# Performance work log

Measured on AMD Instinct MI355X. Metric: run time of the kernel, lower is better.

The kernel has to match this reference:

```python
import jax, jax.numpy as jnp
import numpy as np

# Mamba2 hyperparameters
D_MODEL = 768
D_STATE = 64
D_CONV = 4
EXPAND = 2
HEADDIM = 64
CHUNK = 64
D_INNER = EXPAND * D_MODEL            # 1536
NHEADS = D_INNER // HEADDIM           # 24
D_IN_PROJ = 2 * D_INNER + 2 * D_STATE + NHEADS  # 3224
CONV_DIM = D_INNER + 2 * D_STATE      # 1664
B_SZ = 8
SEQ = 4096  # multiple of CHUNK -> no padding branch


def setup_inputs() -> dict:
    key = jax.random.key(0)
    ks = jax.random.split(key, 6)
    u = jax.random.normal(ks[0], (B_SZ, SEQ, D_MODEL), jnp.float32)
    # fan-in scaled weights (matches nn.Linear/Conv1d default init scale)
    W_in = jax.random.normal(ks[1], (D_IN_PROJ, D_MODEL), jnp.float32) / np.sqrt(D_MODEL).astype(np.float32)
    conv_w = jax.random.normal(ks[2], (CONV_DIM, 1, D_CONV), jnp.float32) / np.sqrt(D_CONV).astype(np.float32)
    conv_b = jnp.zeros((CONV_DIM,), jnp.float32)
    dt_bias = jax.random.uniform(ks[3], (NHEADS,), jnp.float32, -4.0, 1.0)  # nn.init.uniform_(-4, 1)
    A_log = jnp.full((NHEADS,), -np.log(2.0), jnp.float32)                  # nn.init.constant_(-log 2)
    D_param = jnp.ones((NHEADS,), jnp.float32)
    norm_w = jnp.ones((D_INNER,), jnp.float32)
    W_out = jax.random.normal(ks[4], (D_MODEL, D_INNER), jnp.float32) / np.sqrt(D_INNER).astype(np.float32)
    return dict(u=u, W_in=W_in, conv_w=conv_w, conv_b=conv_b, dt_bias=dt_bias,
                A_log=A_log, D_param=D_param, norm_w=norm_w, W_out=W_out)


def _segsum(x):
    """Stable segment sum: out[..., i, j] = sum_{j < k <= i} x[..., k]; -inf above diagonal."""
    T = x.shape[-1]
    lower_strict = jnp.tril(jnp.ones((T, T), bool), -1)
    xe = jnp.where(lower_strict, x[..., :, None], 0.0)   # broadcast x over last (col) axis
    s = jnp.cumsum(xe, axis=-2)
    lower = jnp.tril(jnp.ones((T, T), bool), 0)
    return jnp.where(lower, s, -jnp.inf)


def _ssd(x, A, B, C, chunk):
    """Chunked SSD. x:(b,L,h,p)  A:(b,L,h)  B,C:(b,L,1,n)."""
    b, L, h, p = x.shape
    c = L // chunk
    n = B.shape[-1]
    x = x.reshape(b, c, chunk, h, p)
    A = A.reshape(b, c, chunk, h).transpose(0, 3, 1, 2)   # b h c l
    B = B.reshape(b, c, chunk, 1, n)
    C = C.reshape(b, c, chunk, 1, n)
    A_cs = jnp.cumsum(A, axis=-1)                          # b h c l
    # intra-chunk (diagonal) term
    Lmat = jnp.exp(_segsum(A))                             # b h c l s
    Y_diag = jnp.einsum('bclhn,bcshn,bhcls,bcshp->bclhp', C, B, Lmat, x)
    # per-chunk states
    decay_states = jnp.exp(A_cs[..., -1:] - A_cs)          # b h c l
    states = jnp.einsum('bclhn,bhcl,bclhp->bchpn', B, decay_states, x)
    states = jnp.concatenate([jnp.zeros_like(states[:, :1]), states], axis=1)  # b (c+1) h p n
    # inter-chunk recurrence
    A_last = jnp.pad(A_cs[..., -1], ((0, 0), (0, 0), (1, 0)))  # b h (c+1)
    decay_chunk = jnp.exp(_segsum(A_last))                     # b h (c+1) (c+1)
    new_states = jnp.einsum('bhzc,bchpn->bzhpn', decay_chunk, states)
    states = new_states[:, :-1]                                # b c h p n
    # off-diagonal (state-to-output) term
    Y_off = jnp.einsum('bclhn,bchpn,bhcl->bclhp', C, states, jnp.exp(A_cs))
    return (Y_diag + Y_off).reshape(b, L, h, p)


def reference(u, W_in, conv_w, conv_b, dt_bias, A_log, D_param, norm_w, W_out):
    b, L, _ = u.shape  # L % CHUNK == 0, so pad branch is a no-op
    zxbcdt = u @ W_in.T                                    # (b, L, D_IN_PROJ)
    z = zxbcdt[..., :D_INNER]
    xBC = zxbcdt[..., D_INNER:D_INNER + CONV_DIM]
    dt = jax.nn.softplus(zxbcdt[..., D_INNER + CONV_DIM:] + dt_bias)  # (b, L, h)
    # causal depthwise conv1d (torch pads both sides by d_conv-1 then slices [:L] == left pad)
    xBC = jax.lax.conv_general_dilated(
        xBC.transpose(0, 2, 1), conv_w, window_strides=(1,),
        padding=[(D_CONV - 1, 0)], dimension_numbers=('NCH', 'OIH', 'NCH'),
        feature_group_count=CONV_DIM)
    xBC = jax.nn.silu(xBC.transpose(0, 2, 1) + conv_b)     # (b, L, CONV_DIM)
    x = xBC[..., :D_INNER].reshape(b, L, NHEADS, HEADDIM)
    Bm = xBC[..., D_INNER:D_INNER + D_STATE][:, :, None, :]  # (b, L, 1, n)
    Cm = xBC[..., D_INNER + D_STATE:][:, :, None, :]
    A = -jnp.exp(A_log)                                    # (h,)
    Y = _ssd(x * dt[..., None], A * dt, Bm, Cm, CHUNK)
    y = Y + x * D_param[:, None]                           # skip term
    y = y.reshape(b, L, D_INNER)
    # gated RMSNorm: x * silu(z), then rmsnorm * weight
    y = y * jax.nn.silu(z)
    y = y * jax.lax.rsqrt(jnp.mean(y * y, axis=-1, keepdims=True) + 1e-5) * norm_w
    return y @ W_out.T
```

## Files before the change

### kernel.cpp

```cpp
#include <hip/hip_runtime.h>
#include <stdint.h>

typedef unsigned short u16;
typedef __bf16 bf16x8 __attribute__((ext_vector_type(8)));
typedef float f32x4 __attribute__((ext_vector_type(4)));
typedef unsigned short u16x8 __attribute__((ext_vector_type(8)));
typedef unsigned short u16x4 __attribute__((ext_vector_type(4)));
typedef __attribute__((address_space(1))) unsigned int gu32;
typedef __attribute__((address_space(3))) unsigned int lu32;

__device__ __forceinline__ float bf2f(u16 u){ unsigned int v=((unsigned int)u)<<16; float f; __builtin_memcpy(&f,&v,4); return f; }
__device__ __forceinline__ u16 f2bf(float f){ unsigned int v; __builtin_memcpy(&v,&f,4); v += 0x7fffu + ((v>>16)&1u); return (u16)(v>>16); }
__device__ __forceinline__ void glds16(const void* g, void* l){
  __builtin_amdgcn_global_load_lds((gu32*)g, (lu32*)l, 16, 0, 0);
}

__global__ __launch_bounds__(256) void k_cast(const float* __restrict__ in, u16* __restrict__ out, int n4){
  int i = blockIdx.x*256 + threadIdx.x;
  if (i >= n4) return;
  const f32x4 v = *(const f32x4*)(in + (size_t)i*4);
  u16x4 o; o.x=f2bf(v.x); o.y=f2bf(v.y); o.z=f2bf(v.z); o.w=f2bf(v.w);
  *(u16x4*)(out + (size_t)i*4) = o;
}

__global__ __launch_bounds__(256) void k_cast_pad(const float* __restrict__ in, u16* __restrict__ out){
  int i = blockIdx.x*256 + threadIdx.x;
  int e0 = i*4;
  int row = e0 / 768;
  int col = e0 - row*768;
  u16x4 o;
  if (row < 3224){
    const f32x4 v = *(const f32x4*)(in + (size_t)row*768 + col);
    o.x=f2bf(v.x); o.y=f2bf(v.y); o.z=f2bf(v.z); o.w=f2bf(v.w);
  } else { o.x=0; o.y=0; o.z=0; o.w=0; }
  *(u16x4*)(out + e0) = o;
}

template<int K, int NT, int NH, int EPI>
__global__ __launch_bounds__(256,4) void k_gemm(
    const u16* __restrict__ A, const u16* __restrict__ Bw,
    u16* __restrict__ o_z, u16* __restrict__ o_xbc, float* __restrict__ o_dt,
    const float* __restrict__ dt_bias, float* __restrict__ o_f32)
{
  __shared__ __align__(16) u16 Alds[8192];
  __shared__ __align__(16) u16 Blds[8192];
  const int tid = threadIdx.x;
  const int wave = tid>>6, lane = tid&63;
  constexpr int NPH = NT / NH;
  const int bid = (int)blockIdx.x;
  const int x = bid & 7;
  const int q = bid >> 3;
  const int pass = q / (32*NPH);
  const int rem  = q % (32*NPH);
  const int m0 = ((x<<5) + rem/NPH) << 7;
  const int n0 = (pass*NPH + rem%NPH) << 7;
  const int wr = (wave>>1)<<6, wc = (wave&1)<<6;
  const int srow = tid>>3, sc0 = (tid&7)<<3;
  const int lo16 = lane&15, hi = lane>>4;
  f32x4 acc[4][4] = {};
  for (int k0 = 0; k0 < K; k0 += 64){
    #pragma unroll
    for (int i = 0; i < 4; ++i){
      const int row = (i<<5) + srow;
      const int scol = sc0 ^ ((row&7)<<3);
      glds16(A  + (size_t)(m0+row)*K + k0 + scol, &Alds[(i<<11) + (wave<<9)]);
      glds16(Bw + (size_t)(n0+row)*K + k0 + scol, &Blds[(i<<11) + (wave<<9)]);
    }
    __syncthreads();
    #pragma unroll
    for (int kk = 0; kk < 2; ++kk){
      const int kb = (kk<<5) + (hi<<3);
      bf16x8 af[4], bfv[4];
      #pragma unroll
      for (int m = 0; m < 4; ++m){
        const int r = wr + (m<<4) + lo16;
        af[m] = *(const bf16x8*)&Alds[(r<<6) + (kb ^ ((r&7)<<3))];
      }
      #pragma unroll
      for (int n = 0; n < 4; ++n){
        const int r = wc + (n<<4) + lo16;
        bfv[n] = *(const bf16x8*)&Blds[(r<<6) + (kb ^ ((r&7)<<3))];
      }
      #pragma unroll
      for (int m = 0; m < 4; ++m)
      #pragma unroll
      for (int n = 0; n < 4; ++n)
        acc[m][n] = __builtin_amdgcn_mfma_f32_16x16x32_bf16(af[m], bfv[n], acc[m][n], 0,0,0);
    }
    __syncthreads();
  }
  #pragma unroll
  for (int m = 0; m < 4; ++m)
  #pragma unroll
  for (int n = 0; n < 4; ++n)
  #pragma unroll
  for (int i = 0; i < 4; ++i){
    const int gr = m0 + wr + (m<<4) + (hi<<2) + i;
    const int gc = n0 + wc + (n<<4) + lo16;
    const float v = acc[m][n][i];
    if constexpr (EPI == 0){
      if (gc < 1536)      o_z[(size_t)gr*1536 + gc] = f2bf(v);
      else if (gc < 3200) o_xbc[(size_t)gr*1664 + (gc-1536)] = f2bf(v);
      else if (gc < 3224){
        const float t = v + dt_bias[gc-3200];
        o_dt[(size_t)(gc-3200)*32768 + gr] = (t > 20.f) ? t : log1pf(__expf(t));
      }
    } else {
      o_f32[(size_t)gr*768 + gc] = v;
    }
  }
}

__global__ __launch_bounds__(256) void k_conv(
    const u16* __restrict__ xbc, const float* __restrict__ cw, const float* __restrict__ cb,
    const float* __restrict__ dtT,
    u16* __restrict__ xT, u16* __restrict__ Bn, u16* __restrict__ BT, u16* __restrict__ Cn)
{
  const int idx = blockIdx.x*256 + threadIdx.x;
  if (idx >= 4096*208) return;
  const int g  = idx % 208;
  const int pt = idx / 208;
  const int ch0 = g << 3;
  const int m0 = pt << 3;
  const int l0 = m0 & 4095;
  float wgt[8][4], bias8[8];
  #pragma unroll
  for (int j = 0; j < 8; ++j){
    const f32x4 wv = *(const f32x4*)(cw + (size_t)(ch0+j)*4);
    wgt[j][0]=wv.x; wgt[j][1]=wv.y; wgt[j][2]=wv.z; wgt[j][3]=wv.w;
    bias8[j] = cb[ch0+j];
  }
  float acc[8][8];
  #pragma unroll
  for (int p = 0; p < 8; ++p)
  #pragma unroll
  for (int j = 0; j < 8; ++j) acc[p][j] = bias8[j];
  #pragma unroll
  for (int r = -3; r < 8; ++r){
    const int ls = l0 + r;
    if (ls < 0) continue;
    const u16x8 v = *(const u16x8*)(xbc + (size_t)(m0+r)*1664 + ch0);
    float xf[8];
    #pragma unroll
    for (int j = 0; j < 8; ++j) xf[j] = bf2f(v[j]);
    #pragma unroll
    for (int t = 0; t < 4; ++t){
      const int p = r + 3 - t;
      if (p < 0 || p > 7) continue;
      #pragma unroll
      for (int j = 0; j < 8; ++j) acc[p][j] += xf[j] * wgt[j][t];
    }
  }
  #pragma unroll
  for (int p = 0; p < 8; ++p)
  #pragma unroll
  for (int j = 0; j < 8; ++j){ const float s = acc[p][j]; acc[p][j] = s / (1.f + __expf(-s)); }

  const int b = m0 >> 12;
  const int cch = l0 >> 6;
  const int lr0 = l0 & 63;
  if (ch0 < 1536){
    const int h = ch0 >> 6, p0 = ch0 & 63;
    const f32x4 d0 = *(const f32x4*)(dtT + (size_t)h*32768 + m0);
    const f32x4 d1 = *(const f32x4*)(dtT + (size_t)h*32768 + m0 + 4);
    const float dtl[8] = {d0.x,d0.y,d0.z,d0.w,d1.x,d1.y,d1.z,d1.w};
    const size_t rb = (size_t)(b*24+h)*64;
    #pragma unroll
    for (int j = 0; j < 8; ++j){
      const int row = p0 + j;
      u16x8 o;
      #pragma unroll
      for (int p = 0; p < 8; ++p) o[p] = f2bf(acc[p][j] * dtl[p]);
      *(u16x8*)(xT + (rb + row)*4096 + (size_t)cch*64 + (lr0 ^ ((row&7)<<3))) = o;
    }
  } else if (ch0 < 1600){
    const int n0 = ch0 - 1536;
    const size_t tb = ((size_t)(b*64 + cch))*4096;
    #pragma unroll
    for (int p = 0; p < 8; ++p){
      const int lr = lr0 + p;
      u16x8 o;
      #pragma unroll
      for (int j = 0; j < 8; ++j) o[j] = f2bf(acc[p][j]);
      *(u16x8*)(Bn + tb + lr*64 + (n0 ^ ((lr&7)<<3))) = o;
    }
    #pragma unroll
    for (int j = 0; j < 8; ++j){
      const int row = n0 + j;
      u16x8 o;
      #pragma unroll
      for (int p = 0; p < 8; ++p) o[p] = f2bf(acc[p][j]);
      *(u16x8*)(BT + tb + row*64 + (lr0 ^ ((row&7)<<3))) = o;
    }
  } else {
    const int n0 = ch0 - 1600;
    const size_t tb = ((size_t)(b*64 + cch))*4096;
    #pragma unroll
    for (int p = 0; p < 8; ++p){
      const int lr = lr0 + p;
      u16x8 o;
      #pragma unroll
      for (int j = 0; j < 8; ++j) o[j] = f2bf(acc[p][j]);
      *(u16x8*)(Cn + tb + lr*64 + (n0 ^ ((lr&7)<<3))) = o;
    }
  }
}

__global__ __launch_bounds__(512,1) void k_ssd(
    const u16* __restrict__ xT, const u16* __restrict__ Bn, const u16* __restrict__ BT,
    const u16* __restrict__ Cn, const float* __restrict__ dtT, const float* __restrict__ A_log,
    const float* __restrict__ Dp, u16* __restrict__ yo)
{
  __shared__ __align__(16) u16 tiles[2][4][4096];
  __shared__ __align__(16) u16 Ml[4096];
  __shared__ __align__(16) u16 Sbf[2][4096];
  const int tid = threadIdx.x, wave = tid>>6, lane = tid&63;
  const int sg = wave & 3, hf = wave >> 2;
  const int lo16 = lane&15, hi = lane>>4;
  const int w16 = sg<<4, hi4 = hi<<2;
  const int b = blockIdx.x / 24, h = blockIdx.x % 24;
  const float Ah = -__expf(A_log[h]);
  const float Dh = Dp[h];
  for (int i = tid; i < 8192; i += 512) ((u16*)Sbf)[i] = 0;
  f32x4 Sreg[2] = {};
  const size_t xTg  = (size_t)(b*24+h)*64*4096;
  const size_t bcg  = (size_t)b*64*4096;
  const size_t dtg0 = (size_t)h*32768 + (size_t)b*4096;
  const size_t yb   = (size_t)b*4096*1536 + (size_t)h*64;

  auto stage = [&](int buf, int c){
    u16* dst = &tiles[buf][sg][0];
    if (sg == 0){
      const u16* g0 = xT + xTg + (size_t)c*64 + (size_t)(lane>>3)*4096 + (lane&7)*8;
      #pragma unroll
      for (int s = 0; s < 4; ++s){
        const int sx = (hf<<2) + s;
        glds16(g0 + (size_t)sx*32768, dst + sx*512);
      }
    } else {
      const u16* src = (sg==1 ? Bn : sg==2 ? BT : Cn) + bcg + (size_t)c*4096 + lane*8;
      #pragma unroll
      for (int s = 0; s < 4; ++s){
        const int sx = (hf<<2) + s;
        glds16(src + sx*512, dst + sx*512);
      }
    }
  };

  float dtc = dtT[dtg0 + lane];
  stage(0, 0);

  for (int c = 0; c < 64; ++c){
    float s = Ah * dtc;
    #pragma unroll
    for (int o = 1; o < 64; o <<= 1){ const float t = __shfl_up(s, o); if (lane >= o) s += t; }
    const float Alast = __shfl(s, 63);
    const float lam  = __expf(Alast);
    const float decl = __expf(Alast - s);
    const float elv  = __expf(s);
    float dtn = 0.f;
    if (c < 63){
      dtn = dtT[dtg0 + (size_t)(c+1)*64 + lane];
      stage((c+1)&1, c+1);
    }
    if (c == 0)       asm volatile("s_waitcnt vmcnt(5) lgkmcnt(0)" ::: "memory");
    else if (c == 63) asm volatile("s_waitcnt vmcnt(2) lgkmcnt(0)" ::: "memory");
    else              asm volatile("s_waitcnt vmcnt(7) lgkmcnt(0)" ::: "memory");
    __builtin_amdgcn_s_barrier();

    const u16* tx = &tiles[c&1][0][0];
    const u16* tb = &tiles[c&1][1][0];
    const u16* tt = &tiles[c&1][2][0];
    const u16* tc = &tiles[c&1][3][0];
    const u16* Sr = &Sbf[c&1][0];
    u16*       Sw = &Sbf[(c+1)&1][0];

    f32x4 accG[2] = {};
    bf16x8 bfC[2][2];
    #pragma unroll
    for (int kk = 0; kk < 2; ++kk){
      const int kb = (kk<<5) + (hi<<3);
      const int rA = w16 + lo16;
      const bf16x8 aB = *(const bf16x8*)&tb[(rA<<6) + (kb ^ ((rA&7)<<3))];
      #pragma unroll
      for (int ti = 0; ti < 2; ++ti){
        const int t = (hf<<1) + ti;
        const int rb = (t<<4) + lo16;
        bfC[kk][ti] = *(const bf16x8*)&tc[(rb<<6) + (kb ^ ((rb&7)<<3))];
        accG[ti] = __builtin_amdgcn_mfma_f32_16x16x32_bf16(aB, bfC[kk][ti], accG[ti], 0,0,0);
      }
    }
    float As_i[4];
    #pragma unroll
    for (int i = 0; i < 4; ++i) As_i[i] = __shfl(s, w16 + hi4 + i);
    #pragma unroll
    for (int ti = 0; ti < 2; ++ti){
      const int t = (hf<<1) + ti;
      const int l = (t<<4) + lo16;
      const float Al  = __shfl(s, l);
      const float dtl = __shfl(dtc, l);
      u16x4 ov;
      #pragma unroll
      for (int i = 0; i < 4; ++i){
        const int si = w16 + hi4 + i;
        float v = 0.f;
        if (si <= l) v = accG[ti][i] * __expf(Al - As_i[i]);
        if (si == l) v += Dh / dtl;
        ov[i] = f2bf(v);
      }
      *(u16x4*)&Ml[(l<<6) + ((w16 + hi4) ^ ((l&7)<<3))] = ov;
    }
    asm volatile("s_waitcnt lgkmcnt(0)" ::: "memory");
    __builtin_amdgcn_s_barrier();

    f32x4 aYd[2] = {}, aYo[2] = {}, aS[2] = {};
    #pragma unroll
    for (int kk = 0; kk < 2; ++kk){
      const int kb = (kk<<5) + (hi<<3);
      const int rA = w16 + lo16;
      const int oA = (rA<<6) + (kb ^ ((rA&7)<<3));
      const bf16x8 aX = *(const bf16x8*)&tx[oA];
      const bf16x8 aSb= *(const bf16x8*)&Sr[oA];
      const u16x8 aBTu= *(const u16x8*)&tt[oA];
      u16x8 aBTs;
      #pragma unroll
      for (int j = 0; j < 8; ++j) aBTs[j] = f2bf(bf2f(aBTu[j]) * __shfl(decl, kb + j));
      const bf16x8 aBT = *(const bf16x8*)&aBTs;
      #pragma unroll
      for (int ti = 0; ti < 2; ++ti){
        const int t = (hf<<1) + ti;
        const int rb = (t<<4) + lo16;
        const int o = (rb<<6) + (kb ^ ((rb&7)<<3));
        const bf16x8 bM = *(const bf16x8*)&Ml[o];
        const bf16x8 bX = *(const bf16x8*)&tx[o];
        aYd[ti] = __builtin_amdgcn_mfma_f32_16x16x32_bf16(aX,  bM,         aYd[ti], 0,0,0);
        aYo[ti] = __builtin_amdgcn_mfma_f32_16x16x32_bf16(aSb, bfC[kk][ti], aYo[ti], 0,0,0);
        aS[ti]  = __builtin_amdgcn_mfma_f32_16x16x32_bf16(aBT, bX,         aS[ti],  0,0,0);
      }
    }
    #pragma unroll
    for (int ti = 0; ti < 2; ++ti){
      const int t = (hf<<1) + ti;
      const int p = (t<<4) + lo16;
      u16x4 sv;
      #pragma unroll
      for (int i = 0; i < 4; ++i){
        const float nv = Sreg[ti][i] * lam + aS[ti][i];
        Sreg[ti][i] = nv;
        sv[i] = f2bf(nv);
      }
      *(u16x4*)&Sw[(p<<6) + ((w16 + hi4) ^ ((p&7)<<3))] = sv;
    }
    #pragma unroll
    for (int ti = 0; ti < 2; ++ti){
      const int t = (hf<<1) + ti;
      const int l = (t<<4) + lo16;
      const float elt = __shfl(elv, l);
      u16x4 ov;
      #pragma unroll
      for (int i = 0; i < 4; ++i) ov[i] = f2bf(aYd[ti][i] + elt * aYo[ti][i]);
      *(u16x4*)(yo + yb + (size_t)((c<<6)+l)*1536 + w16 + hi4) = ov;
    }
    dtc = dtn;
  }
}

__global__ __launch_bounds__(192) void k_gnorm(
    const u16* __restrict__ y, const u16* __restrict__ z,
    const float* __restrict__ nw, u16* __restrict__ out)
{
  __shared__ float red[3];
  const int m = blockIdx.x, t = threadIdx.x;
  const size_t base = (size_t)m*1536 + t*8;
  const u16x8 yv = *(const u16x8*)(y + base);
  const u16x8 zv = *(const u16x8*)(z + base);
  float vals[8]; float ss = 0.f;
  #pragma unroll
  for (int j = 0; j < 8; ++j){
    const float zf = bf2f(zv[j]);
    const float v = bf2f(yv[j]) * zf / (1.f + __expf(-zf));
    vals[j] = v; ss += v*v;
  }
  #pragma unroll
  for (int off = 32; off > 0; off >>= 1) ss += __shfl_down(ss, off);
  if ((t & 63) == 0) red[t>>6] = ss;
  __syncthreads();
  const float sc = rsqrtf((red[0]+red[1]+red[2]) * (1.f/1536.f) + 1e-5f);
  u16x8 o;
  #pragma unroll
  for (int j = 0; j < 8; ++j) o[j] = f2bf(vals[j] * sc * nw[t*8+j]);
  *(u16x8*)(out + base) = o;
}

extern "C" void kernel_launch(void* const* d_in, const int* in_sizes, int n_in,
                              void* d_out, int out_size, void* d_ws, size_t ws_size,
                              hipStream_t stream)
{
  const float* u       = (const float*)d_in[0];
  const float* W_in    = (const float*)d_in[1];
  const float* conv_w  = (const float*)d_in[2];
  const float* conv_b  = (const float*)d_in[3];
  const float* dt_bias = (const float*)d_in[4];
  const float* A_log   = (const float*)d_in[5];
  const float* D_param = (const float*)d_in[6];
  const float* norm_w  = (const float*)d_in[7];
  const float* W_out   = (const float*)d_in[8];
  (void)in_sizes; (void)n_in; (void)out_size;
  if (ws_size < (size_t)379715584) return;

  char* w = (char*)d_ws;
  size_t off = 0;
  auto alloc = [&](size_t bytes)->void*{ void* p = w + off; off += (bytes + 255) & ~(size_t)255; return p; };
  u16* ubf    = (u16*)alloc(50331648);
  u16* winbf  = (u16*)alloc(5111808);
  u16* woutbf = (u16*)alloc(2359296);
  u16* zbf    = (u16*)alloc(100663296);
  u16* xbcbf  = (u16*)alloc(109051904);
  float* dtT  = (float*)alloc(3145728);
  u16* xTb    = (u16*)alloc(100663296);
  u16* Bnb    = (u16*)alloc(4194304);
  u16* Cnb    = (u16*)alloc(4194304);
  u16* BTb    = ubf;
  u16* yssd   = xbcbf;
  u16* ynorm  = xTb;

  k_cast<<<24576, 256, 0, stream>>>(u, ubf, 6291456);
  k_cast_pad<<<2496, 256, 0, stream>>>(W_in, winbf);
  k_cast<<<1152, 256, 0, stream>>>(W_out, woutbf, 294912);
  k_gemm<768,26,2,0><<<6656, 256, 0, stream>>>(ubf, winbf, zbf, xbcbf, dtT, dt_bias, nullptr);
  k_conv<<<3328, 256, 0, stream>>>(xbcbf, conv_w, conv_b, dtT, xTb, Bnb, BTb, Cnb);
  k_ssd<<<192, 512, 0, stream>>>(xTb, Bnb, BTb, Cnb, dtT, A_log, D_param, yssd);
  k_gnorm<<<32768, 192, 0, stream>>>(yssd, zbf, norm_w, ynorm);
  k_gemm<1536,6,1,1><<<1536, 256, 0, stream>>>(ynorm, woutbf, nullptr, nullptr, nullptr, nullptr, (float*)d_out);
}
```

Measured before the change: 638.2 us.

## Fuse gated RMSNorm into SSD epilogue and out-projection GEMM row scaling

Removes the separate gated-norm kernel. The SSD epilogue now loads z, applies the silu gate and writes per-head partial sums of squares. A small kernel reduces these to per-row rsqrt scales, which the output GEMM epilogue applies, while norm_w is folded into the bf16 W_out cast. This saves a full read and write pass over the 100MB activation, at the cost of extra z loads and LDS traffic inside the latency-bound SSD loop, plus adjusted waitcnt counts.

```diff
diff --git a/kernel.cpp b/kernel.cpp
--- a/kernel.cpp
+++ b/kernel.cpp
@@ -34,6 +34,26 @@
     o.x=f2bf(v.x); o.y=f2bf(v.y); o.z=f2bf(v.z); o.w=f2bf(v.w);
   } else { o.x=0; o.y=0; o.z=0; o.w=0; }
   *(u16x4*)(out + e0) = o;
+}
+
+__global__ __launch_bounds__(256) void k_cast_wout(const float* __restrict__ in, const float* __restrict__ nw, u16* __restrict__ out){
+  int i = blockIdx.x*256 + threadIdx.x;
+  if (i >= 294912) return;
+  const int e0 = i*4;
+  const int k = e0 % 1536;
+  const f32x4 v = *(const f32x4*)(in + e0);
+  const f32x4 w4 = *(const f32x4*)(nw + k);
+  u16x4 o; o.x=f2bf(v.x*w4.x); o.y=f2bf(v.y*w4.y); o.z=f2bf(v.z*w4.z); o.w=f2bf(v.w*w4.w);
+  *(u16x4*)(out + e0) = o;
+}
+
+__global__ __launch_bounds__(256) void k_scale(const float* __restrict__ ps, float* __restrict__ sc){
+  const int m = blockIdx.x*256 + threadIdx.x;
+  const float* p = ps + (size_t)m*24;
+  float s = 0.f;
+  #pragma unroll
+  for (int j = 0; j < 6; ++j){ const f32x4 v = *(const f32x4*)(p + j*4); s += v.x+v.y+v.z+v.w; }
+  sc[m] = rsqrtf(s*(1.f/1536.f) + 1e-5f);
 }
 
 template<int K, int NT, int NH, int EPI>
@@ -106,7 +126,7 @@
         o_dt[(size_t)(gc-3200)*32768 + gr] = (t > 20.f) ? t : log1pf(__expf(t));
       }
     } else {
-      o_f32[(size_t)gr*768 + gc] = v;
+      o_f32[(size_t)gr*768 + gc] = v * o_dt[gr];
     }
   }
 }
@@ -209,11 +229,13 @@
 __global__ __launch_bounds__(512,1) void k_ssd(
     const u16* __restrict__ xT, const u16* __restrict__ Bn, const u16* __restrict__ BT,
     const u16* __restrict__ Cn, const float* __restrict__ dtT, const float* __restrict__ A_log,
-    const float* __restrict__ Dp, u16* __restrict__ yo)
+    const float* __restrict__ Dp, const u16* __restrict__ zg, float* __restrict__ psum,
+    u16* __restrict__ yo)
 {
   __shared__ __align__(16) u16 tiles[2][4][4096];
   __shared__ __align__(16) u16 Ml[4096];
   __shared__ __align__(16) u16 Sbf[2][4096];
+  __shared__ float ps_lds[2][64][4];
   const int tid = threadIdx.x, wave = tid>>6, lane = tid&63;
   const int sg = wave & 3, hf = wave >> 2;
   const int lo16 = lane&15, hi = lane>>4;
@@ -227,6 +249,7 @@
   const size_t bcg  = (size_t)b*64*4096;
   const size_t dtg0 = (size_t)h*32768 + (size_t)b*4096;
   const size_t yb   = (size_t)b*4096*1536 + (size_t)h*64;
+  const size_t pbase = (size_t)b*4096*24 + h;
 
   auto stage = [&](int buf, int c){
     u16* dst = &tiles[buf][sg][0];
@@ -251,6 +274,12 @@
   stage(0, 0);
 
   for (int c = 0; c < 64; ++c){
+    u16x4 zv[2];
+    #pragma unroll
+    for (int ti = 0; ti < 2; ++ti){
+      const int l = (((hf<<1)+ti)<<4) + lo16;
+      zv[ti] = *(const u16x4*)(zg + yb + (size_t)((c<<6)+l)*1536 + w16 + hi4);
+    }
     float s = Ah * dtc;
     #pragma unroll
     for (int o = 1; o < 64; o <<= 1){ const float t = __shfl_up(s, o); if (lane >= o) s += t; }
@@ -263,10 +292,15 @@
       dtn = dtT[dtg0 + (size_t)(c+1)*64 + lane];
       stage((c+1)&1, c+1);
     }
-    if (c == 0)       asm volatile("s_waitcnt vmcnt(5) lgkmcnt(0)" ::: "memory");
-    else if (c == 63) asm volatile("s_waitcnt vmcnt(2) lgkmcnt(0)" ::: "memory");
-    else              asm volatile("s_waitcnt vmcnt(7) lgkmcnt(0)" ::: "memory");
+    if (c == 0)       asm volatile("s_waitcnt vmcnt(6) lgkmcnt(0)" ::: "memory");
+    else if (c == 63) asm volatile("s_waitcnt vmcnt(3) lgkmcnt(0)" ::: "memory");
+    else              asm volatile("s_waitcnt vmcnt(8) lgkmcnt(0)" ::: "memory");
     __builtin_amdgcn_s_barrier();
+
+    if (wave == 7 && c > 0){
+      const f32x4 pv = *(const f32x4*)&ps_lds[(c&1)^1][lane][0];
+      psum[pbase + (size_t)(((c-1)<<6) + lane)*24] = pv.x+pv.y+pv.z+pv.w;
+    }
 
     const u16* tx = &tiles[c&1][0][0];
     const u16* tb = &tiles[c&1][1][0];
@@ -357,39 +391,27 @@
       const int l = (t<<4) + lo16;
       const float elt = __shfl(elv, l);
       u16x4 ov;
-      #pragma unroll
-      for (int i = 0; i < 4; ++i) ov[i] = f2bf(aYd[ti][i] + elt * aYo[ti][i]);
+      float pss = 0.f;
+      #pragma unroll
+      for (int i = 0; i < 4; ++i){
+        const float zf = bf2f(zv[ti][i]);
+        const float yg = (aYd[ti][i] + elt * aYo[ti][i]) * (zf / (1.f + __expf(-zf)));
+        ov[i] = f2bf(yg);
+        pss += yg * yg;
+      }
       *(u16x4*)(yo + yb + (size_t)((c<<6)+l)*1536 + w16 + hi4) = ov;
+      pss += __shfl_xor(pss, 16);
+      pss += __shfl_xor(pss, 32);
+      if (hi == 0) ps_lds[c&1][l][sg] = pss;
     }
     dtc = dtn;
   }
-}
-
-__global__ __launch_bounds__(192) void k_gnorm(
-    const u16* __restrict__ y, const u16* __restrict__ z,
-    const float* __restrict__ nw, u16* __restrict__ out)
-{
-  __shared__ float red[3];
-  const int m = blockIdx.x, t = threadIdx.x;
-  const size_t base = (size_t)m*1536 + t*8;
-  const u16x8 yv = *(const u16x8*)(y + base);
-  const u16x8 zv = *(const u16x8*)(z + base);
-  float vals[8]; float ss = 0.f;
-  #pragma unroll
-  for (int j = 0; j < 8; ++j){
-    const float zf = bf2f(zv[j]);
-    const float v = bf2f(yv[j]) * zf / (1.f + __expf(-zf));
-    vals[j] = v; ss += v*v;
-  }
-  #pragma unroll
-  for (int off = 32; off > 0; off >>= 1) ss += __shfl_down(ss, off);
-  if ((t & 63) == 0) red[t>>6] = ss;
-  __syncthreads();
-  const float sc = rsqrtf((red[0]+red[1]+red[2]) * (1.f/1536.f) + 1e-5f);
-  u16x8 o;
-  #pragma unroll
-  for (int j = 0; j < 8; ++j) o[j] = f2bf(vals[j] * sc * nw[t*8+j]);
-  *(u16x8*)(out + base) = o;
+  asm volatile("s_waitcnt lgkmcnt(0)" ::: "memory");
+  __builtin_amdgcn_s_barrier();
+  if (wave == 7){
+    const f32x4 pv = *(const f32x4*)&ps_lds[1][lane][0];
+    psum[pbase + (size_t)((63<<6) + lane)*24] = pv.x+pv.y+pv.z+pv.w;
+  }
 }
 
 extern "C" void kernel_launch(void* const* d_in, const int* in_sizes, int n_in,
@@ -421,15 +443,16 @@
   u16* Bnb    = (u16*)alloc(4194304);
   u16* Cnb    = (u16*)alloc(4194304);
   u16* BTb    = ubf;
-  u16* yssd   = xbcbf;
-  u16* ynorm  = xTb;
+  u16* yg     = xbcbf;
+  float* psum = (float*)winbf;
+  float* scbuf= (float*)(w + 50331648 + ((3145728 + 255) & ~(size_t)255));
 
   k_cast<<<24576, 256, 0, stream>>>(u, ubf, 6291456);
   k_cast_pad<<<2496, 256, 0, stream>>>(W_in, winbf);
-  k_cast<<<1152, 256, 0, stream>>>(W_out, woutbf, 294912);
+  k_cast_wout<<<1152, 256, 0, stream>>>(W_out, norm_w, woutbf);
   k_gemm<768,26,2,0><<<6656, 256, 0, stream>>>(ubf, winbf, zbf, xbcbf, dtT, dt_bias, nullptr);
   k_conv<<<3328, 256, 0, stream>>>(xbcbf, conv_w, conv_b, dtT, xTb, Bnb, BTb, Cnb);
-  k_ssd<<<192, 512, 0, stream>>>(xTb, Bnb, BTb, Cnb, dtT, A_log, D_param, yssd);
-  k_gnorm<<<32768, 192, 0, stream>>>(yssd, zbf, norm_w, ynorm);
-  k_gemm<1536,6,1,1><<<1536, 256, 0, stream>>>(ynorm, woutbf, nullptr, nullptr, nullptr, nullptr, (float*)d_out);
-}
+  k_ssd<<<192, 512, 0, stream>>>(xTb, Bnb, BTb, Cnb, dtT, A_log, D_param, zbf, psum, yg);
+  k_scale<<<128, 256, 0, stream>>>(psum, scbuf);
+  k_gemm<1536,6,1,1><<<1536, 256, 0, stream>>>(yg, woutbf, nullptr, nullptr, scbuf, nullptr, (float*)d_out);
+}
```

Result: no change. 645.7 us (+1.2%).
